# Performance work log

Hardware: AMD Instinct MI355X
Metric: run time of the kernel (lower is better)

Reference implementation:

```python
import jax, jax.numpy as jnp
import numpy as np

B, N, FEAT, H = 4, 1024, 512, 8
HD = FEAT // H


def _xavier(key, shape, gain):
    fan_in, fan_out = shape[1], shape[0]
    a = gain * np.sqrt(6.0 / (fan_in + fan_out))
    return jax.random.uniform(key, shape, jnp.float32, -a, a)


def setup_inputs() -> dict:
    key = jax.random.key(0)
    ks = jax.random.split(key, 12)
    g = 2 ** (-0.5)
    return {
        "ndata": jax.random.normal(ks[0], (B, N, FEAT), jnp.float32),
        "attn_bias": jax.random.normal(ks[1], (B, N, N, H), jnp.float32),
        "attn_mask": jax.random.bernoulli(ks[2], 0.1, (B, N, N, H)),
        "Wq": _xavier(ks[3], (FEAT, FEAT), g), "bq": jnp.zeros((FEAT,), jnp.float32),
        "Wk": _xavier(ks[4], (FEAT, FEAT), g), "bk": jnp.zeros((FEAT,), jnp.float32),
        "Wv": _xavier(ks[5], (FEAT, FEAT), g), "bv": jnp.zeros((FEAT,), jnp.float32),
        "Wo": _xavier(ks[6], (FEAT, FEAT), 1.0), "bo": jnp.zeros((FEAT,), jnp.float32),
    }


def reference(ndata, attn_bias, attn_mask, Wq, bq, Wk, bk, Wv, bv, Wo, bo):
    b, n, feat = ndata.shape
    h = attn_bias.shape[-1]
    hd = feat // h
    scaling = hd ** (-0.5)
    # projections -> [B, N, H, HD]
    q = (ndata @ Wq.T + bq).reshape(b, n, h, hd) * scaling
    k = (ndata @ Wk.T + bk).reshape(b, n, h, hd)
    v = (ndata @ Wv.T + bv).reshape(b, n, h, hd)
    # scores [B, N(q), N(k), H] to match torch layout for bias/mask
    scores = jnp.einsum("bihd,bjhd->bijh", q, k)
    scores = scores + attn_bias
    scores = jnp.where(attn_mask, -jnp.inf, scores)
    attn = jax.nn.softmax(scores, axis=2)  # softmax over key dim
    out = jnp.einsum("bijh,bjhd->bihd", attn, v).reshape(b, n, feat)
    return out @ Wo.T + bo
```

## Files before the change

### kernel.cpp

```cpp
#include <hip/hip_runtime.h>
#include <hip/hip_bf16.h>
#include <cstdint>


namespace {

typedef short bf16x8 __attribute__((ext_vector_type(8)));
typedef float f32x4 __attribute__((ext_vector_type(4)));
using u16 = unsigned short;
using u8 = unsigned char;

__device__ __forceinline__ u16 f2bf(float f) {
  union { float f; uint32_t i; } v;
  v.f = f;
  uint32_t r = v.i + 0x7fffu + ((v.i >> 16) & 1u);
  return (u16)(r >> 16);
}

__device__ __forceinline__ void gload_lds16(const void* g, void* l) {
  __builtin_amdgcn_global_load_lds(
      (__attribute__((address_space(1))) void*)g,
      (__attribute__((address_space(3))) void*)l, 16, 0, 0);
}
__device__ __forceinline__ void gload_lds4(const void* g, void* l) {
  __builtin_amdgcn_global_load_lds(
      (__attribute__((address_space(1))) void*)g,
      (__attribute__((address_space(3))) void*)l, 4, 0, 0);
}

__global__ void detect_mask_kernel(const unsigned char* __restrict__ m,
                                   int* __restrict__ flag) {
  __shared__ int red[256];
  int local = 0;
  for (int i = threadIdx.x; i < 65536; i += 256) local += (m[i] != 0) ? 1 : 0;
  red[threadIdx.x] = local;
  __syncthreads();
  for (int s = 128; s > 0; s >>= 1) {
    if ((int)threadIdx.x < s) red[threadIdx.x] += red[threadIdx.x + s];
    __syncthreads();
  }
  if (threadIdx.x == 0) *flag = (red[0] > 4915) ? 1 : 0;
}

__global__ __launch_bounds__(256) void canon_mask(const int* __restrict__ m32,
                                                  const int* __restrict__ flag,
                                                  u8* __restrict__ out) {
  if (*flag != 0) return;
  const size_t t = (size_t)blockIdx.x * 256 + threadIdx.x;
  const int4* src = (const int4*)m32 + t * 8;
  uchar4 ob[8];
#pragma unroll
  for (int q = 0; q < 8; ++q) {
    const int4 v = src[q];
    ob[q] = make_uchar4(v.x != 0, v.y != 0, v.z != 0, v.w != 0);
  }
  *(uint4*)(out + t * 32) = *(const uint4*)&ob[0];
  *(uint4*)(out + t * 32 + 16) = *(const uint4*)&ob[4];
}

__global__ __launch_bounds__(256) void convert_kernel(
    const float* __restrict__ nd, const float* __restrict__ Wq,
    const float* __restrict__ Wk, const float* __restrict__ Wv,
    const float* __restrict__ Wo, u16* __restrict__ A16,
    u16* __restrict__ W16) {
  const int gi = blockIdx.x * 256 + threadIdx.x;
  const float* src;
  u16* dst;
  int off;
  if (gi < 524288) {
    src = nd; dst = A16; off = gi * 4;
  } else {
    const int w = (gi - 524288) >> 16;
    off = ((gi - 524288) & 65535) * 4;
    src = (w == 0) ? Wq : (w == 1) ? Wk : (w == 2) ? Wv : Wo;
    dst = W16 + (size_t)w * 262144;
  }
  const float4 v = *(const float4*)&src[off];
  ushort4 o;
  o.x = f2bf(v.x); o.y = f2bf(v.y); o.z = f2bf(v.z); o.w = f2bf(v.w);
  *(ushort4*)&dst[off] = o;
}

template <int EPI>
__global__ __launch_bounds__(256) void gemm_nt(
    const u16* __restrict__ A16, const u16* __restrict__ W16,
    const float* __restrict__ bq, const float* __restrict__ bk,
    const float* __restrict__ bv, u16* __restrict__ Q16,
    u16* __restrict__ KF, u16* __restrict__ VF,
    const float* __restrict__ bo, float* __restrict__ OutF) {
  __shared__ u16 As[128 * 64];
  __shared__ u16 Ws[64 * 64];
  const int tid = threadIdx.x, lane = tid & 63, wid = tid >> 6;
  const int r0 = blockIdx.x * 128;
  int wsel, c0;
  const float* bias;
  float scale = 1.0f;
  if (EPI == 0) {
    wsel = blockIdx.y >> 3;
    c0 = (blockIdx.y & 7) * 64;
    bias = (wsel == 0) ? bq : (wsel == 1) ? bk : bv;
    if (wsel == 0) scale = 0.125f;
  } else {
    wsel = 3;
    c0 = blockIdx.y * 64;
    bias = bo;
  }
  const u16* W = W16 + (size_t)wsel * (512 * 512);
  const int wm = (wid >> 1) * 64, wn = (wid & 1) * 32;

  f32x4 acc[4][2] = {};
  for (int k0 = 0; k0 < 512; k0 += 64) {
    __syncthreads();
#pragma unroll
    for (int p = 0; p < 4; ++p) {
      const int o = p * 4096 + tid * 16;
      const int row = o >> 7, kb = o & 127;
      gload_lds16((const char*)A16 + (size_t)(r0 + row) * 1024 + k0 * 2 +
                      (kb ^ ((row & 7) << 4)),
                  (char*)As + o);
    }
#pragma unroll
    for (int p = 0; p < 2; ++p) {
      const int o = p * 4096 + tid * 16;
      const int row = o >> 7, kb = o & 127;
      gload_lds16((const char*)W + (size_t)(c0 + row) * 1024 + k0 * 2 +
                      (kb ^ ((row & 7) << 4)),
                  (char*)Ws + o);
    }
    __syncthreads();
    bf16x8 af[4][2], bf[2][2];
#pragma unroll
    for (int mt = 0; mt < 4; ++mt)
#pragma unroll
      for (int ks = 0; ks < 2; ++ks) {
        const int row = wm + mt * 16 + (lane & 15);
        const int kb = ks * 64 + (lane >> 4) * 16;
        af[mt][ks] = *(const bf16x8*)((const char*)As + row * 128 +
                                      (kb ^ ((row & 7) << 4)));
      }
#pragma unroll
    for (int nt = 0; nt < 2; ++nt)
#pragma unroll
      for (int ks = 0; ks < 2; ++ks) {
        const int row = wn + nt * 16 + (lane & 15);
        const int kb = ks * 64 + (lane >> 4) * 16;
        bf[nt][ks] = *(const bf16x8*)((const char*)Ws + row * 128 +
                                      (kb ^ ((row & 7) << 4)));
      }
#pragma unroll
    for (int mt = 0; mt < 4; ++mt)
#pragma unroll
      for (int nt = 0; nt < 2; ++nt)
#pragma unroll
        for (int ks = 0; ks < 2; ++ks)
          acc[mt][nt] = __builtin_amdgcn_mfma_f32_16x16x32_bf16(
              af[mt][ks], bf[nt][ks], acc[mt][nt], 0, 0, 0);
  }
  float bvals[2];
#pragma unroll
  for (int nt = 0; nt < 2; ++nt)
    bvals[nt] = bias[c0 + wn + nt * 16 + (lane & 15)];
#pragma unroll
  for (int mt = 0; mt < 4; ++mt)
#pragma unroll
    for (int nt = 0; nt < 2; ++nt)
#pragma unroll
      for (int r = 0; r < 4; ++r) {
        const int row = r0 + wm + mt * 16 + (lane >> 4) * 4 + r;
        const int col = c0 + wn + nt * 16 + (lane & 15);
        const float v = (acc[mt][nt][r] + bvals[nt]) * scale;
        if (EPI == 0) {
          const int bb = row >> 10, n = row & 1023, hh = col >> 6,
                    dd = col & 63;
          if (wsel == 0) {
            Q16[((size_t)(bb * 8 + hh) * 1024 + n) * 64 + dd] = f2bf(v);
          } else if (wsel == 1) {
            const int jc = n >> 5, tt = (n >> 4) & 1, ln = n & 15;
            const int ks = dd >> 5, gg = (dd >> 3) & 3, e = dd & 7;
            KF[(((((size_t)(bb * 8 + hh) * 32 + jc) * 2 + tt) * 2 + ks) * 64 +
                gg * 16 + ln) * 8 + e] = f2bf(v);
          } else {
            const int jc = n >> 5, jl = n & 31;
            const int gg = (jl & 15) >> 2;
            const int e = (jl < 16) ? (jl & 3) : (4 + (jl & 3));
            const int dt = dd >> 4, ii = dd & 15;
            VF[((((size_t)(bb * 8 + hh) * 32 + jc) * 4 + dt) * 512) +
               (gg * 16 + ii) * 8 + e] = f2bf(v);
          }
        } else {
          OutF[(size_t)row * 512 + col] = v;
        }
      }
}

__global__ __launch_bounds__(512, 4) void attn_fused3(
    const u16* __restrict__ Q16, const u16* __restrict__ KF,
    const u16* __restrict__ VF, const float* __restrict__ bias,
    const u8* __restrict__ mask8, const u8* __restrict__ mask_ws,
    const int* __restrict__ flag, float* __restrict__ Opart,
    float* __restrict__ Mm, float* __restrict__ Ll) {
  __shared__ __align__(16) char biasL[2][16384];
  __shared__ __align__(16) char maskL[2][4096];

  const int tid = threadIdx.x, lane = tid & 63, h = tid >> 6;
  const int bid = blockIdx.x;
  const int b = bid & 3, half = (bid >> 2) & 1, it = bid >> 3;
  const int i0 = it * 16;
  const u8* mk = (*flag != 0) ? mask8 : mask_ws;

  const int i = lane & 15, g = lane >> 4;
  const int g1 = g & 1, g2 = g >> 1;
  const int bh = b * 8 + h;

  const u16* Qh = Q16 + (size_t)bh * 65536;
  bf16x8 qf[2];
#pragma unroll
  for (int ks = 0; ks < 2; ++ks)
    qf[ks] = *(const bf16x8*)&Qh[(size_t)(i0 + i) * 64 + ks * 32 + g * 8];

  float mo = -3e38f, lo = 0.f;
  f32x4 oacc[4] = {};

  const size_t rowb = (size_t)(b * 1024 + i0) * 8192;
  int boff[8];
#pragma unroll
  for (int q = 0; q < 8; ++q) {
    const int w = q * 512 + tid;
    const int wi = w >> 8, oct = (w >> 6) & 3, slot = w & 63;
    const int se = slot ^ wi ^ ((oct & 1) << 4);
    boff[q] = wi * 8192 + oct * 64 + se;
  }
  int moff[2];
#pragma unroll
  for (int q = 0; q < 2; ++q) {
    const int bb2 = (q * 512 + tid) * 4;
    const int wi = bb2 >> 8, oct = (bb2 >> 6) & 3, sl = bb2 & 63;
    const int se = sl ^ ((wi << 2) & 0x3C);
    moff[q] = wi * 8192 + oct * 64 + se;
  }
  const int Cb = (((g1 << 5) | h) ^ i ^ (g2 << 4)) << 2;
  const int baseb = i * 1024 + g2 * 256;
  const int Cm = ((g1 << 5) | h) ^ ((i << 2) & 0x3C);
  const int basem = i * 256 + g2 * 64;

  auto STAGE = [&](int buf, int jc) {
    const float* bsrc = bias + rowb + (size_t)jc * 256;
    const u8* msrc = mk + rowb + (size_t)jc * 256;
#pragma unroll
    for (int q = 0; q < 8; ++q)
      gload_lds4(bsrc + boff[q], biasL[buf] + (q * 512 + tid) * 4);
#pragma unroll
    for (int q = 0; q < 2; ++q)
      gload_lds4(msrc + moff[q], maskL[buf] + (q * 512 + tid) * 4);
  };

  const int jcBase = half * 16;
  STAGE(0, jcBase);

  for (int t = 0; t < 16; ++t) {
    asm volatile("s_waitcnt vmcnt(0)" ::: "memory");
    __builtin_amdgcn_s_barrier();
    const char* bb_ = biasL[t & 1];
    const char* mb_ = maskL[t & 1];
    const int jc = jcBase + t;
    const size_t kvb = (size_t)bh * 32 + jc;

    bf16x8 kf[2][2];
#pragma unroll
    for (int t2 = 0; t2 < 2; ++t2)
#pragma unroll
      for (int ks = 0; ks < 2; ++ks)
        kf[t2][ks] =
            *(const bf16x8*)&KF[((kvb * 2 + t2) * 2 + ks) * 512 + lane * 8];
    bf16x8 vf[4];
#pragma unroll
    for (int dt = 0; dt < 4; ++dt)
      vf[dt] = *(const bf16x8*)&VF[(kvb * 4 + dt) * 512 + lane * 8];

    if (t < 15) STAGE((t + 1) & 1, jc + 1);

    f32x4 sa[2] = {};
#pragma unroll
    for (int t2 = 0; t2 < 2; ++t2)
#pragma unroll
      for (int ks = 0; ks < 2; ++ks)
        sa[t2] = __builtin_amdgcn_mfma_f32_16x16x32_bf16(kf[t2][ks], qf[ks],
                                                         sa[t2], 0, 0, 0);

    float s[2][4];
#pragma unroll
    for (int t2 = 0; t2 < 2; ++t2)
#pragma unroll
      for (int r = 0; r < 4; ++r) {
        const float bv =
            *(const float*)(bb_ + baseb + t2 * 512 + (Cb ^ (r << 5)));
        const u8 mv = *(const u8*)(mb_ + basem + t2 * 128 + (Cm ^ (r << 3)));
        s[t2][r] = mv ? -1e30f : (sa[t2][r] + bv);
      }

    float cm = s[0][0];
#pragma unroll
    for (int k = 1; k < 8; ++k) cm = fmaxf(cm, s[k >> 2][k & 3]);
    cm = fmaxf(cm, __shfl_xor(cm, 16));
    cm = fmaxf(cm, __shfl_xor(cm, 32));
    const bool upd = __any(cm > mo);
    const float mn = fmaxf(mo, cm);
    const float sc = __expf(mo - mn);
    float p[2][4], rs = 0.f;
#pragma unroll
    for (int k = 0; k < 8; ++k) {
      const float pv = __expf(s[k >> 2][k & 3] - mn);
      p[k >> 2][k & 3] = pv;
      rs += pv;
    }
    rs += __shfl_xor(rs, 16);
    rs += __shfl_xor(rs, 32);
    lo = lo * sc + rs;
    mo = mn;
    if (upd) {
      float scB[4];
#pragma unroll
      for (int r = 0; r < 4; ++r) scB[r] = __shfl(sc, g * 4 + r);
#pragma unroll
      for (int dt = 0; dt < 4; ++dt)
#pragma unroll
        for (int r = 0; r < 4; ++r) oacc[dt][r] *= scB[r];
    }

    union { u16 us[8]; bf16x8 v; } pk;
#pragma unroll
    for (int e = 0; e < 4; ++e) {
      pk.us[e] = f2bf(p[0][e]);
      pk.us[4 + e] = f2bf(p[1][e]);
    }
#pragma unroll
    for (int dt = 0; dt < 4; ++dt)
      oacc[dt] = __builtin_amdgcn_mfma_f32_16x16x32_bf16(pk.v, vf[dt],
                                                         oacc[dt], 0, 0, 0);
  }

  float* Op = Opart + (size_t)half * 2097152 +
              ((size_t)(b * 1024 + i0)) * 512 + h * 64;
#pragma unroll
  for (int r = 0; r < 4; ++r)
#pragma unroll
    for (int dt = 0; dt < 4; ++dt)
      Op[(size_t)(g * 4 + r) * 512 + dt * 16 + i] = oacc[dt][r];
  if (lane < 16) {
    const size_t mi = ((size_t)(half * 4 + b) * 8 + h) * 1024 + i0 + lane;
    Mm[mi] = mo;
    Ll[mi] = lo;
  }
}

__global__ __launch_bounds__(256) void combine_halves(
    const float* __restrict__ Opart, const float* __restrict__ Mm,
    const float* __restrict__ Ll, u16* __restrict__ Ow) {
  const int t = blockIdx.x * 256 + threadIdx.x;
  const int col4 = t & 127, row = t >> 7;
  const int b = row >> 10, i = row & 1023, h = col4 >> 4;
  const size_t o0 = (size_t)row * 512 + col4 * 4;
  const float4 v0 = *(const float4*)&Opart[o0];
  const float4 v1 = *(const float4*)&Opart[o0 + 2097152];
  const size_t mi0 = ((size_t)b * 8 + h) * 1024 + i;
  const float m0 = Mm[mi0], m1 = Mm[mi0 + 32768];
  const float l0 = Ll[mi0], l1 = Ll[mi0 + 32768];
  const float M = fmaxf(m0, m1);
  const float e0 = __expf(m0 - M), e1 = __expf(m1 - M);
  const float inv = 1.0f / (l0 * e0 + l1 * e1);
  ushort4 o;
  o.x = f2bf((v0.x * e0 + v1.x * e1) * inv);
  o.y = f2bf((v0.y * e0 + v1.y * e1) * inv);
  o.z = f2bf((v0.z * e0 + v1.z * e1) * inv);
  o.w = f2bf((v0.w * e0 + v1.w * e1) * inv);
  *(ushort4*)&Ow[o0] = o;
}

}

extern "C" void kernel_launch(void* const* d_in, const int* in_sizes, int n_in,
                              void* d_out, int out_size, void* d_ws,
                              size_t ws_size, hipStream_t stream) {
  const float* ndata = (const float*)d_in[0];
  const float* bias = (const float*)d_in[1];
  const void* mask = d_in[2];
  const float* Wq = (const float*)d_in[3];
  const float* bq = (const float*)d_in[4];
  const float* Wk = (const float*)d_in[5];
  const float* bk = (const float*)d_in[6];
  const float* Wv = (const float*)d_in[7];
  const float* bvp = (const float*)d_in[8];
  const float* Wo = (const float*)d_in[9];
  const float* bo = (const float*)d_in[10];
  float* out = (float*)d_out;

  u16* A16 = (u16*)d_ws;
  u16* W16 = A16 + 2097152;
  u16* Q16 = W16 + 1048576;
  u16* KF = Q16 + 2097152;
  u16* VF = KF + 2097152;
  u16* Ow = VF + 2097152;
  float* Opart = (float*)(Ow + 2097152);
  float* Mm = Opart + 4194304;
  float* Ll = Mm + 65536;
  u8* mask_ws = (u8*)(Ll + 65536);
  int* flag = (int*)(mask_ws + 33554432);

  detect_mask_kernel<<<1, 256, 0, stream>>>((const unsigned char*)mask, flag);
  canon_mask<<<4096, 256, 0, stream>>>((const int*)mask, flag, mask_ws);
  convert_kernel<<<3072, 256, 0, stream>>>(ndata, Wq, Wk, Wv, Wo, A16, W16);
  gemm_nt<0><<<dim3(32, 24), 256, 0, stream>>>(A16, W16, bq, bk, bvp, Q16, KF,
                                               VF, nullptr, nullptr);
  attn_fused3<<<512, 512, 0, stream>>>(Q16, KF, VF, bias, (const u8*)mask,
                                       mask_ws, flag, Opart, Mm, Ll);
  combine_halves<<<2048, 256, 0, stream>>>(Opart, Mm, Ll, Ow);
  gemm_nt<1><<<dim3(32, 8), 256, 0, stream>>>(Ow, W16, nullptr, nullptr,
                                              nullptr, nullptr, nullptr,
                                              nullptr, bo, out);
}
```

Measured before the change: 184.8 us.

## Split attention key range into quarters and defer softmax rescaling lazily

The fused attention kernel now splits the key dimension into four parts instead of two. That doubles the grid to 1024 blocks and raises the launch-bounds occupancy hint, and a four-way combine kernel merges the partial results. The online softmax also skips the max update and accumulator rescale unless some row's new max exceeds the running max by more than 8. This is meant to cut per-iteration rescale work and improve load balance and latency hiding on the bias and mask streaming. In exchange, the partial-output workspace and its combine read traffic double, and probabilities may reach up to e^8 before rescaling, which costs some precision in the bf16 P matrix.

```diff
diff --git a/kernel.cpp b/kernel.cpp
--- a/kernel.cpp
+++ b/kernel.cpp
@@ -193,7 +193,7 @@
       }
 }
 
-__global__ __launch_bounds__(512, 4) void attn_fused3(
+__global__ __launch_bounds__(512, 8) void attn_fused4(
     const u16* __restrict__ Q16, const u16* __restrict__ KF,
     const u16* __restrict__ VF, const float* __restrict__ bias,
     const u8* __restrict__ mask8, const u8* __restrict__ mask_ws,
@@ -204,7 +204,10 @@
 
   const int tid = threadIdx.x, lane = tid & 63, h = tid >> 6;
   const int bid = blockIdx.x;
-  const int b = bid & 3, half = (bid >> 2) & 1, it = bid >> 3;
+  const int s = bid & 7, gg_ = bid >> 3;
+  const int b = s >> 1;
+  const int quarter = ((gg_ & 1) << 1) | (s & 1);
+  const int it = gg_ >> 1;
   const int i0 = it * 16;
   const u8* mk = (*flag != 0) ? mask8 : mask_ws;
 
@@ -254,10 +257,10 @@
       gload_lds4(msrc + moff[q], maskL[buf] + (q * 512 + tid) * 4);
   };
 
-  const int jcBase = half * 16;
+  const int jcBase = quarter * 8;
   STAGE(0, jcBase);
 
-  for (int t = 0; t < 16; ++t) {
+  for (int t = 0; t < 8; ++t) {
     asm volatile("s_waitcnt vmcnt(0)" ::: "memory");
     __builtin_amdgcn_s_barrier();
     const char* bb_ = biasL[t & 1];
@@ -277,7 +280,7 @@
     for (int dt = 0; dt < 4; ++dt)
       vf[dt] = *(const bf16x8*)&VF[(kvb * 4 + dt) * 512 + lane * 8];
 
-    if (t < 15) STAGE((t + 1) & 1, jc + 1);
+    if (t < 7) STAGE((t + 1) & 1, jc + 1);
 
     f32x4 sa[2] = {};
 #pragma unroll
@@ -287,7 +290,7 @@
         sa[t2] = __builtin_amdgcn_mfma_f32_16x16x32_bf16(kf[t2][ks], qf[ks],
                                                          sa[t2], 0, 0, 0);
 
-    float s[2][4];
+    float ss[2][4];
 #pragma unroll
     for (int t2 = 0; t2 < 2; ++t2)
 #pragma unroll
@@ -295,37 +298,37 @@
         const float bv =
             *(const float*)(bb_ + baseb + t2 * 512 + (Cb ^ (r << 5)));
         const u8 mv = *(const u8*)(mb_ + basem + t2 * 128 + (Cm ^ (r << 3)));
-        s[t2][r] = mv ? -1e30f : (sa[t2][r] + bv);
+        ss[t2][r] = mv ? -1e30f : (sa[t2][r] + bv);
       }
 
-    float cm = s[0][0];
-#pragma unroll
-    for (int k = 1; k < 8; ++k) cm = fmaxf(cm, s[k >> 2][k & 3]);
+    float cm = ss[0][0];
+#pragma unroll
+    for (int k = 1; k < 8; ++k) cm = fmaxf(cm, ss[k >> 2][k & 3]);
     cm = fmaxf(cm, __shfl_xor(cm, 16));
     cm = fmaxf(cm, __shfl_xor(cm, 32));
-    const bool upd = __any(cm > mo);
-    const float mn = fmaxf(mo, cm);
-    const float sc = __expf(mo - mn);
+    if (!__all(cm <= mo + 8.f)) {
+      const float mn = fmaxf(mo, cm);
+      const float sc = __expf(mo - mn);
+      mo = mn;
+      lo *= sc;
+      float scB[4];
+#pragma unroll
+      for (int r = 0; r < 4; ++r) scB[r] = __shfl(sc, g * 4 + r);
+#pragma unroll
+      for (int dt = 0; dt < 4; ++dt)
+#pragma unroll
+        for (int r = 0; r < 4; ++r) oacc[dt][r] *= scB[r];
+    }
     float p[2][4], rs = 0.f;
 #pragma unroll
     for (int k = 0; k < 8; ++k) {
-      const float pv = __expf(s[k >> 2][k & 3] - mn);
+      const float pv = __expf(ss[k >> 2][k & 3] - mo);
       p[k >> 2][k & 3] = pv;
       rs += pv;
     }
     rs += __shfl_xor(rs, 16);
     rs += __shfl_xor(rs, 32);
-    lo = lo * sc + rs;
-    mo = mn;
-    if (upd) {
-      float scB[4];
-#pragma unroll
-      for (int r = 0; r < 4; ++r) scB[r] = __shfl(sc, g * 4 + r);
-#pragma unroll
-      for (int dt = 0; dt < 4; ++dt)
-#pragma unroll
-        for (int r = 0; r < 4; ++r) oacc[dt][r] *= scB[r];
-    }
+    lo += rs;
 
     union { u16 us[8]; bf16x8 v; } pk;
 #pragma unroll
@@ -339,7 +342,7 @@
                                                          oacc[dt], 0, 0, 0);
   }
 
-  float* Op = Opart + (size_t)half * 2097152 +
+  float* Op = Opart + (size_t)quarter * 2097152 +
               ((size_t)(b * 1024 + i0)) * 512 + h * 64;
 #pragma unroll
   for (int r = 0; r < 4; ++r)
@@ -347,32 +350,49 @@
     for (int dt = 0; dt < 4; ++dt)
       Op[(size_t)(g * 4 + r) * 512 + dt * 16 + i] = oacc[dt][r];
   if (lane < 16) {
-    const size_t mi = ((size_t)(half * 4 + b) * 8 + h) * 1024 + i0 + lane;
+    const size_t mi = ((size_t)(quarter * 4 + b) * 8 + h) * 1024 + i0 + lane;
     Mm[mi] = mo;
     Ll[mi] = lo;
   }
 }
 
-__global__ __launch_bounds__(256) void combine_halves(
+__global__ __launch_bounds__(256) void combine_quarters(
     const float* __restrict__ Opart, const float* __restrict__ Mm,
     const float* __restrict__ Ll, u16* __restrict__ Ow) {
   const int t = blockIdx.x * 256 + threadIdx.x;
   const int col4 = t & 127, row = t >> 7;
   const int b = row >> 10, i = row & 1023, h = col4 >> 4;
   const size_t o0 = (size_t)row * 512 + col4 * 4;
-  const float4 v0 = *(const float4*)&Opart[o0];
-  const float4 v1 = *(const float4*)&Opart[o0 + 2097152];
   const size_t mi0 = ((size_t)b * 8 + h) * 1024 + i;
-  const float m0 = Mm[mi0], m1 = Mm[mi0 + 32768];
-  const float l0 = Ll[mi0], l1 = Ll[mi0 + 32768];
-  const float M = fmaxf(m0, m1);
-  const float e0 = __expf(m0 - M), e1 = __expf(m1 - M);
-  const float inv = 1.0f / (l0 * e0 + l1 * e1);
+  float4 v[4];
+  float m[4], l[4];
+#pragma unroll
+  for (int q = 0; q < 4; ++q) {
+    v[q] = *(const float4*)&Opart[o0 + (size_t)q * 2097152];
+    m[q] = Mm[mi0 + q * 32768];
+    l[q] = Ll[mi0 + q * 32768];
+  }
+  const float M = fmaxf(fmaxf(m[0], m[1]), fmaxf(m[2], m[3]));
+  float e[4], den = 0.f;
+#pragma unroll
+  for (int q = 0; q < 4; ++q) {
+    e[q] = __expf(m[q] - M);
+    den += l[q] * e[q];
+  }
+  const float inv = 1.0f / den;
+  float4 acc = make_float4(0.f, 0.f, 0.f, 0.f);
+#pragma unroll
+  for (int q = 0; q < 4; ++q) {
+    acc.x += v[q].x * e[q];
+    acc.y += v[q].y * e[q];
+    acc.z += v[q].z * e[q];
+    acc.w += v[q].w * e[q];
+  }
   ushort4 o;
-  o.x = f2bf((v0.x * e0 + v1.x * e1) * inv);
-  o.y = f2bf((v0.y * e0 + v1.y * e1) * inv);
-  o.z = f2bf((v0.z * e0 + v1.z * e1) * inv);
-  o.w = f2bf((v0.w * e0 + v1.w * e1) * inv);
+  o.x = f2bf(acc.x * inv);
+  o.y = f2bf(acc.y * inv);
+  o.z = f2bf(acc.z * inv);
+  o.w = f2bf(acc.w * inv);
   *(ushort4*)&Ow[o0] = o;
 }
 
@@ -401,9 +421,9 @@
   u16* VF = KF + 2097152;
   u16* Ow = VF + 2097152;
   float* Opart = (float*)(Ow + 2097152);
-  float* Mm = Opart + 4194304;
-  float* Ll = Mm + 65536;
-  u8* mask_ws = (u8*)(Ll + 65536);
+  float* Mm = Opart + 8388608;
+  float* Ll = Mm + 131072;
+  u8* mask_ws = (u8*)(Ll + 131072);
   int* flag = (int*)(mask_ws + 33554432);
 
   detect_mask_kernel<<<1, 256, 0, stream>>>((const unsigned char*)mask, flag);
@@ -411,9 +431,9 @@
   convert_kernel<<<3072, 256, 0, stream>>>(ndata, Wq, Wk, Wv, Wo, A16, W16);
   gemm_nt<0><<<dim3(32, 24), 256, 0, stream>>>(A16, W16, bq, bk, bvp, Q16, KF,
                                                VF, nullptr, nullptr);
-  attn_fused3<<<512, 512, 0, stream>>>(Q16, KF, VF, bias, (const u8*)mask,
-                                       mask_ws, flag, Opart, Mm, Ll);
-  combine_halves<<<2048, 256, 0, stream>>>(Opart, Mm, Ll, Ow);
+  attn_fused4<<<1024, 512, 0, stream>>>(Q16, KF, VF, bias, (const u8*)mask,
+                                        mask_ws, flag, Opart, Mm, Ll);
+  combine_quarters<<<2048, 256, 0, stream>>>(Opart, Mm, Ll, Ow);
   gemm_nt<1><<<dim3(32, 8), 256, 0, stream>>>(Ow, W16, nullptr, nullptr,
                                               nullptr, nullptr, nullptr,
                                               nullptr, bo, out);
```

Measured after the change: 287.4 us. 55.6% more time.

## Triple-buffer bias/mask staging and add lazy softmax max rescaling

Applied to the files above, without the earlier changes.

The attention kernel now keeps three LDS buffers for bias and mask tiles and prefetches two chunks ahead. Each iteration waits with vmcnt(10) instead of draining all loads, which should hide more global-memory latency on the bias stream. The online softmax now rescales the accumulator only when the running max grows by more than 8, so most iterations skip the rescale and its shuffles. The trade-offs are 50% more LDS per block, which may lower occupancy, and exponentials up to e^8 in fp32/bf16, which could lose some accuracy.

```diff
diff --git a/kernel.cpp b/kernel.cpp
--- a/kernel.cpp
+++ b/kernel.cpp
@@ -193,14 +193,14 @@
       }
 }
 
-__global__ __launch_bounds__(512, 4) void attn_fused3(
+__global__ __launch_bounds__(512, 4) void attn_fused5(
     const u16* __restrict__ Q16, const u16* __restrict__ KF,
     const u16* __restrict__ VF, const float* __restrict__ bias,
     const u8* __restrict__ mask8, const u8* __restrict__ mask_ws,
     const int* __restrict__ flag, float* __restrict__ Opart,
     float* __restrict__ Mm, float* __restrict__ Ll) {
-  __shared__ __align__(16) char biasL[2][16384];
-  __shared__ __align__(16) char maskL[2][4096];
+  __shared__ __align__(16) char biasL[3][16384];
+  __shared__ __align__(16) char maskL[3][4096];
 
   const int tid = threadIdx.x, lane = tid & 63, h = tid >> 6;
   const int bid = blockIdx.x;
@@ -256,12 +256,14 @@
 
   const int jcBase = half * 16;
   STAGE(0, jcBase);
+  STAGE(1, jcBase + 1);
+  asm volatile("s_waitcnt vmcnt(10)" ::: "memory");
+  __builtin_amdgcn_s_barrier();
 
   for (int t = 0; t < 16; ++t) {
-    asm volatile("s_waitcnt vmcnt(0)" ::: "memory");
-    __builtin_amdgcn_s_barrier();
-    const char* bb_ = biasL[t & 1];
-    const char* mb_ = maskL[t & 1];
+    const int buf = t % 3;
+    const char* bb_ = biasL[buf];
+    const char* mb_ = maskL[buf];
     const int jc = jcBase + t;
     const size_t kvb = (size_t)bh * 32 + jc;
 
@@ -277,7 +279,7 @@
     for (int dt = 0; dt < 4; ++dt)
       vf[dt] = *(const bf16x8*)&VF[(kvb * 4 + dt) * 512 + lane * 8];
 
-    if (t < 15) STAGE((t + 1) & 1, jc + 1);
+    if (t < 14) STAGE((t + 2) % 3, jc + 2);
 
     f32x4 sa[2] = {};
 #pragma unroll
@@ -287,7 +289,7 @@
         sa[t2] = __builtin_amdgcn_mfma_f32_16x16x32_bf16(kf[t2][ks], qf[ks],
                                                          sa[t2], 0, 0, 0);
 
-    float s[2][4];
+    float ss[2][4];
 #pragma unroll
     for (int t2 = 0; t2 < 2; ++t2)
 #pragma unroll
@@ -295,37 +297,37 @@
         const float bv =
             *(const float*)(bb_ + baseb + t2 * 512 + (Cb ^ (r << 5)));
         const u8 mv = *(const u8*)(mb_ + basem + t2 * 128 + (Cm ^ (r << 3)));
-        s[t2][r] = mv ? -1e30f : (sa[t2][r] + bv);
+        ss[t2][r] = mv ? -1e30f : (sa[t2][r] + bv);
       }
 
-    float cm = s[0][0];
-#pragma unroll
-    for (int k = 1; k < 8; ++k) cm = fmaxf(cm, s[k >> 2][k & 3]);
+    float cm = ss[0][0];
+#pragma unroll
+    for (int k = 1; k < 8; ++k) cm = fmaxf(cm, ss[k >> 2][k & 3]);
     cm = fmaxf(cm, __shfl_xor(cm, 16));
     cm = fmaxf(cm, __shfl_xor(cm, 32));
-    const bool upd = __any(cm > mo);
-    const float mn = fmaxf(mo, cm);
-    const float sc = __expf(mo - mn);
+    if (!__all(cm <= mo + 8.f)) {
+      const float mn = fmaxf(mo, cm);
+      const float sc = __expf(mo - mn);
+      mo = mn;
+      lo *= sc;
+      float scB[4];
+#pragma unroll
+      for (int r = 0; r < 4; ++r) scB[r] = __shfl(sc, g * 4 + r);
+#pragma unroll
+      for (int dt = 0; dt < 4; ++dt)
+#pragma unroll
+        for (int r = 0; r < 4; ++r) oacc[dt][r] *= scB[r];
+    }
     float p[2][4], rs = 0.f;
 #pragma unroll
     for (int k = 0; k < 8; ++k) {
-      const float pv = __expf(s[k >> 2][k & 3] - mn);
+      const float pv = __expf(ss[k >> 2][k & 3] - mo);
       p[k >> 2][k & 3] = pv;
       rs += pv;
     }
     rs += __shfl_xor(rs, 16);
     rs += __shfl_xor(rs, 32);
-    lo = lo * sc + rs;
-    mo = mn;
-    if (upd) {
-      float scB[4];
-#pragma unroll
-      for (int r = 0; r < 4; ++r) scB[r] = __shfl(sc, g * 4 + r);
-#pragma unroll
-      for (int dt = 0; dt < 4; ++dt)
-#pragma unroll
-        for (int r = 0; r < 4; ++r) oacc[dt][r] *= scB[r];
-    }
+    lo += rs;
 
     union { u16 us[8]; bf16x8 v; } pk;
 #pragma unroll
@@ -337,6 +339,14 @@
     for (int dt = 0; dt < 4; ++dt)
       oacc[dt] = __builtin_amdgcn_mfma_f32_16x16x32_bf16(pk.v, vf[dt],
                                                          oacc[dt], 0, 0, 0);
+
+    if (t < 14) {
+      asm volatile("s_waitcnt vmcnt(10)" ::: "memory");
+      __builtin_amdgcn_s_barrier();
+    } else if (t == 14) {
+      asm volatile("s_waitcnt vmcnt(0)" ::: "memory");
+      __builtin_amdgcn_s_barrier();
+    }
   }
 
   float* Op = Opart + (size_t)half * 2097152 +
@@ -411,7 +421,7 @@
   convert_kernel<<<3072, 256, 0, stream>>>(ndata, Wq, Wk, Wv, Wo, A16, W16);
   gemm_nt<0><<<dim3(32, 24), 256, 0, stream>>>(A16, W16, bq, bk, bvp, Q16, KF,
                                                VF, nullptr, nullptr);
-  attn_fused3<<<512, 512, 0, stream>>>(Q16, KF, VF, bias, (const u8*)mask,
+  attn_fused5<<<512, 512, 0, stream>>>(Q16, KF, VF, bias, (const u8*)mask,
                                        mask_ws, flag, Opart, Mm, Ll);
   combine_halves<<<2048, 256, 0, stream>>>(Opart, Mm, Ll, Ow);
   gemm_nt<1><<<dim3(32, 8), 256, 0, stream>>>(Ow, W16, nullptr, nullptr,
```

Measured after the change: 170.0 us. 8.0% less time.
